# Kernel optimization log

Measured on AMD Instinct MI355X. Metric: run time of the kernel, lower is better.

## Reference

```python
import jax, jax.numpy as jnp
import numpy as np

EMPTY, TRUE, FALSE = 0.0, 1.0, 2.0  # MemoryVal ternary encoding

B = 2048          # batch
IN_BITS = 4096    # raw input bits
N_IN, N_ST, N_OUT = 2048, 1024, 1024
K = 14            # bits (connections) per neuron -> memory_size = 2**K
M = 2 ** K


def setup_inputs() -> dict:
    key = jax.random.key(0)
    ks = jax.random.split(key, 8)
    return {
        "input_bits": jax.random.randint(ks[0], (B, IN_BITS), 0, 2, dtype=jnp.int32),
        "state_bits": jax.random.randint(ks[1], (B, N_ST), 0, 2, dtype=jnp.int32),
        "in_conn": jax.random.randint(ks[2], (N_IN, K), 0, IN_BITS, dtype=jnp.int32),
        "in_mem": jax.random.randint(ks[3], (N_IN, M), 0, 3).astype(jnp.float32),
        "st_conn": jax.random.randint(ks[4], (N_ST, K), 0, N_IN + N_ST, dtype=jnp.int32),
        "st_mem": jax.random.randint(ks[5], (N_ST, M), 0, 3).astype(jnp.float32),
        "out_conn": jax.random.randint(ks[6], (N_OUT, K), 0, N_IN + N_ST, dtype=jnp.int32),
        "out_mem": jax.random.randint(ks[7], (N_OUT, M), 0, 3).astype(jnp.float32),
    }


def _ram_layer(bits, conn, mem):
    """bits: [B, T] 0/1; conn: [N, K] indices into T; mem: [N, 2**K] ternary."""
    k = conn.shape[1]
    g = bits[:, conn].astype(jnp.int32)                      # [B, N, K] gathered local bits
    w = (2 ** jnp.arange(k - 1, -1, -1)).astype(jnp.int32)   # MSB-first packing (matches _get_desired_bits)
    addr = jnp.sum(g * w, axis=-1)                           # [B, N] memory addresses
    vals = mem[jnp.arange(mem.shape[0])[None, :], addr]      # [B, N] per-neuron LUT lookup
    return jnp.where(vals == TRUE, 1.0, 0.0).astype(jnp.float32)  # neuron fires iff TRUE


def reference(input_bits, state_bits, in_conn, in_mem, st_conn, st_mem, out_conn, out_mem):
    h_in = _ram_layer(input_bits, in_conn, in_mem)                          # [B, N_IN]
    s_inp = jnp.concatenate([h_in, state_bits.astype(h_in.dtype)], axis=1)  # [B, N_IN+N_ST]
    s_out = _ram_layer(s_inp, st_conn, st_mem)                              # [B, N_ST]
    o_inp = jnp.concatenate([h_in, s_out], axis=1)                          # [B, N_IN+N_ST]
    return _ram_layer(o_inp, out_conn, out_mem)                             # [B, N_OUT]
```

## Files before the change

### kernel.cpp

```cpp
#include <hip/hip_runtime.h>
#include <stdint.h>

#define BATCH   2048
#define IN_BITS 4096
#define N_IN    2048
#define N_ST    1024
#define N_OUT   1024
#define KBITS   14
#define MW      512

#define BROW 128
#define PAD  129

#define IM_F 33554432L
#define SM_F 16777216L
#define OM_F 16777216L

__global__ __launch_bounds__(256) void pack_mem(const float* __restrict__ im,
                                                const float* __restrict__ sm,
                                                const float* __restrict__ om,
                                                uint32_t* __restrict__ dst) {
    int wid = (blockIdx.x * 256 + threadIdx.x) >> 6;
    int lane = threadIdx.x & 63;
    long f0 = (long)wid << 10;
    const float* s;
    long base;
    if (f0 < IM_F)              { s = im; base = f0; }
    else if (f0 < IM_F + SM_F)  { s = sm; base = f0 - IM_F; }
    else                        { s = om; base = f0 - (IM_F + SM_F); }
    unsigned long long m[16];
#pragma unroll
    for (int j = 0; j < 16; j++)
        m[j] = __ballot(s[base + j * 64 + lane] == 1.0f);
    if (lane == 0) {
        uint4* o = (uint4*)(dst + (f0 >> 5));
#pragma unroll
        for (int j = 0; j < 8; j++) {
            uint4 q;
            q.x = (uint32_t)m[2 * j];
            q.y = (uint32_t)(m[2 * j] >> 32);
            q.z = (uint32_t)m[2 * j + 1];
            q.w = (uint32_t)(m[2 * j + 1] >> 32);
            o[j] = q;
        }
    }
}

__global__ __launch_bounds__(256) void pack_in(const int* __restrict__ src,
                                               uint32_t* __restrict__ dst) {
    int wid = (blockIdx.x * 256 + threadIdx.x) >> 6;
    int lane = threadIdx.x & 63;
    long f0 = (long)wid << 10;
    unsigned long long m[16];
#pragma unroll
    for (int j = 0; j < 16; j++)
        m[j] = __ballot(src[f0 + j * 64 + lane] == 1);
    if (lane == 0) {
        uint4* o = (uint4*)(dst + (f0 >> 5));
#pragma unroll
        for (int j = 0; j < 8; j++) {
            uint4 q;
            q.x = (uint32_t)m[2 * j];
            q.y = (uint32_t)(m[2 * j] >> 32);
            q.z = (uint32_t)m[2 * j + 1];
            q.w = (uint32_t)(m[2 * j + 1] >> 32);
            o[j] = q;
        }
    }
}

__global__ __launch_bounds__(256) void pack_st(const int* __restrict__ src,
                                               uint32_t* __restrict__ buf) {
    int wid = (blockIdx.x * 256 + threadIdx.x) >> 6;
    int lane = threadIdx.x & 63;
    long f0 = (long)wid << 10;
    unsigned long long m[16];
#pragma unroll
    for (int j = 0; j < 16; j++)
        m[j] = __ballot(src[f0 + j * 64 + lane] == 1);
    if (lane == 0) {
        uint4* o = (uint4*)(buf + (long)wid * BROW + 64);
#pragma unroll
        for (int j = 0; j < 8; j++) {
            uint4 q;
            q.x = (uint32_t)m[2 * j];
            q.y = (uint32_t)(m[2 * j] >> 32);
            q.z = (uint32_t)m[2 * j + 1];
            q.w = (uint32_t)(m[2 * j + 1] >> 32);
            o[j] = q;
        }
    }
}

template <int NW, int MODE>
__global__ __launch_bounds__(256) void ram_layer(const uint32_t* __restrict__ src,
                                                 const int* __restrict__ conn,
                                                 const uint32_t* __restrict__ memp,
                                                 uint32_t* __restrict__ dst) {
    __shared__ uint32_t lds[64 * PAD];
    const int tid = threadIdx.x;
    const int b0 = blockIdx.y * 64;

    {
        const uint4* g = (const uint4*)(src + (long)b0 * BROW);
        for (int v = tid; v < 64 * BROW / 4; v += 256) {
            uint4 d = g[v];
            int row = v >> 5;
            int col = (v & 31) * 4;
            uint32_t* p = lds + row * PAD + col;
            p[0] = d.x; p[1] = d.y; p[2] = d.z; p[3] = d.w;
        }
    }
    __syncthreads();

    const int lane = tid & 63;
    const int wv = __builtin_amdgcn_readfirstlane(tid >> 6);
    const int n0 = blockIdx.x * (4 * NW) + wv * NW;
    const uint32_t* myrow = lds + lane * PAD;

    unsigned long long msk = 0;
#pragma unroll 2
    for (int i = 0; i < NW; ++i) {
        const int n = n0 + i;
        const int* c = conn + n * KBITS;
        uint32_t addr = 0;
#pragma unroll
        for (int k = 0; k < KBITS; k++) {
            int idx = c[k];
            int wd = idx >> 5;
            if (MODE == 2 && idx >= 2048) wd += 32;
            addr = (addr << 1) | ((myrow[wd] >> (idx & 31)) & 1u);
        }
        uint32_t v = memp[(long)n * MW + (addr >> 5)];
        unsigned long long m = __ballot(((v >> (addr & 31)) & 1u) != 0);
        msk = (lane == i) ? m : msk;
    }

    unsigned long long x = msk;
#define TSTEP(S, M)                                                         \
    {                                                                       \
        unsigned long long t =                                              \
            (unsigned long long)__shfl_xor((long long)x, S, 64);            \
        x = (lane & S) ? ((x & ~(M)) | ((t & ~(M)) >> S))                   \
                       : ((x & (M)) | ((t & (M)) << S));                    \
    }
    TSTEP(32, 0x00000000ffffffffULL)
    TSTEP(16, 0x0000ffff0000ffffULL)
    TSTEP(8,  0x00ff00ff00ff00ffULL)
    TSTEP(4,  0x0f0f0f0f0f0f0f0fULL)
    TSTEP(2,  0x3333333333333333ULL)
    TSTEP(1,  0x5555555555555555ULL)
#undef TSTEP

    if (MODE == 0) {
        *(uint32_t*)(dst + (long)(b0 + lane) * BROW + (n0 >> 5)) = (uint32_t)x;
    } else if (MODE == 1) {
        ((uint16_t*)(dst + (long)(b0 + lane) * BROW + 96))[n0 >> 4] = (uint16_t)x;
    } else {
        ((uint16_t*)(dst + (long)(b0 + lane) * 32))[n0 >> 4] = (uint16_t)x;
    }
}

__global__ __launch_bounds__(256) void expand_out(const uint32_t* __restrict__ pout,
                                                  float4* __restrict__ out) {
    int t = blockIdx.x * 256 + threadIdx.x;
    int b = t >> 8;
    int c4 = (t & 255) * 4;
    uint32_t w = pout[b * 32 + (c4 >> 5)];
    int sh = c4 & 31;
    float4 f;
    f.x = (float)((w >> (sh + 0)) & 1u);
    f.y = (float)((w >> (sh + 1)) & 1u);
    f.z = (float)((w >> (sh + 2)) & 1u);
    f.w = (float)((w >> (sh + 3)) & 1u);
    out[t] = f;
}

extern "C" void kernel_launch(void* const* d_in, const int* in_sizes, int n_in,
                              void* d_out, int out_size, void* d_ws, size_t ws_size,
                              hipStream_t stream) {
    const int*   input_bits = (const int*)d_in[0];
    const int*   state_bits = (const int*)d_in[1];
    const int*   in_conn    = (const int*)d_in[2];
    const float* in_mem     = (const float*)d_in[3];
    const int*   st_conn    = (const int*)d_in[4];
    const float* st_mem     = (const float*)d_in[5];
    const int*   out_conn   = (const int*)d_in[6];
    const float* out_mem    = (const float*)d_in[7];
    float*       out        = (float*)d_out;

    char* ws = (char*)d_ws;
    uint32_t* bits1 = (uint32_t*)(ws);
    uint32_t* buf   = (uint32_t*)(ws + 1048576);
    uint32_t* pout  = (uint32_t*)(ws + 2097152);
    uint32_t* tbl   = (uint32_t*)(ws + 2359296);
    uint32_t* im_p  = tbl;
    uint32_t* sm_p  = tbl + 1048576;
    uint32_t* om_p  = tbl + 1572864;

    pack_in<<<2048, 256, 0, stream>>>(input_bits, bits1);
    pack_st<<<512, 256, 0, stream>>>(state_bits, buf);
    pack_mem<<<16384, 256, 0, stream>>>(in_mem, st_mem, out_mem, tbl);

    ram_layer<32, 0><<<dim3(16, 32), 256, 0, stream>>>(bits1, in_conn, im_p, buf);
    ram_layer<16, 1><<<dim3(16, 32), 256, 0, stream>>>(buf, st_conn, sm_p, buf);
    ram_layer<16, 2><<<dim3(16, 32), 256, 0, stream>>>(buf, out_conn, om_p, pout);

    expand_out<<<2048, 256, 0, stream>>>(pout, (float4*)out);
}
```

Measured before the change: 370.9 us.

## Fuse pack kernels with vectorized loads, halve per-wave neurons, fold output expansion

Merges the three pack kernels into one launch that reads inputs and memory tables with 16-byte vector loads and combines nibbles through lane shuffles instead of per-element ballots. Each RAM layer now uses half as many neurons per wave over a grid twice as wide, which gives more blocks for occupancy. The last layer writes float outputs directly, removing the separate expand kernel and the packed output buffer. The packing stage is dominated by reading the large float memory tables, so it stays bandwidth-bound. The narrower ballots still use only the low lanes (16 and 8 bits), so the bit-transpose does redundant work.

```diff
diff --git a/kernel.cpp b/kernel.cpp
--- a/kernel.cpp
+++ b/kernel.cpp
@@ -2,92 +2,82 @@
 #include <stdint.h>
 
 #define BATCH   2048
-#define IN_BITS 4096
-#define N_IN    2048
-#define N_ST    1024
-#define N_OUT   1024
 #define KBITS   14
 #define MW      512
-
-#define BROW 128
-#define PAD  129
+#define BROW    128
+#define PAD     129
 
 #define IM_F 33554432L
 #define SM_F 16777216L
-#define OM_F 16777216L
 
-__global__ __launch_bounds__(256) void pack_mem(const float* __restrict__ im,
-                                                const float* __restrict__ sm,
-                                                const float* __restrict__ om,
-                                                uint32_t* __restrict__ dst) {
-    int wid = (blockIdx.x * 256 + threadIdx.x) >> 6;
-    int lane = threadIdx.x & 63;
-    long f0 = (long)wid << 10;
-    const float* s;
-    long base;
-    if (f0 < IM_F)              { s = im; base = f0; }
-    else if (f0 < IM_F + SM_F)  { s = sm; base = f0 - IM_F; }
-    else                        { s = om; base = f0 - (IM_F + SM_F); }
-    unsigned long long m[16];
+#define W_IN  4096
+#define W_ST  5120
+#define W_END 37888
+
+__global__ __launch_bounds__(256) void pack_all(
+    const int4* __restrict__ in_b, const int4* __restrict__ st_b,
+    const float4* __restrict__ im, const float4* __restrict__ sm,
+    const float4* __restrict__ om,
+    uint32_t* __restrict__ bits1, uint32_t* __restrict__ buf,
+    uint32_t* __restrict__ tbl) {
+    const int gw = (blockIdx.x * 256 + threadIdx.x) >> 6;
+    const int lane = threadIdx.x & 63;
+    uint32_t nib[8];
+    long wbase;
+    if (gw < W_ST) {
+        const int4* src;
+        long ebase;
+        if (gw < W_IN) { src = in_b; ebase = (long)gw << 11; }
+        else           { src = st_b; ebase = (long)(gw - W_IN) << 11; }
+        const int4* p = src + (ebase >> 2) + lane;
+        int4 r[8];
 #pragma unroll
-    for (int j = 0; j < 16; j++)
-        m[j] = __ballot(s[base + j * 64 + lane] == 1.0f);
-    if (lane == 0) {
-        uint4* o = (uint4*)(dst + (f0 >> 5));
+        for (int j = 0; j < 8; j++) r[j] = p[j * 64];
 #pragma unroll
-        for (int j = 0; j < 8; j++) {
-            uint4 q;
-            q.x = (uint32_t)m[2 * j];
-            q.y = (uint32_t)(m[2 * j] >> 32);
-            q.z = (uint32_t)m[2 * j + 1];
-            q.w = (uint32_t)(m[2 * j + 1] >> 32);
-            o[j] = q;
-        }
+        for (int j = 0; j < 8; j++)
+            nib[j] = (uint32_t)(r[j].x == 1) | ((uint32_t)(r[j].y == 1) << 1) |
+                     ((uint32_t)(r[j].z == 1) << 2) | ((uint32_t)(r[j].w == 1) << 3);
+        wbase = ebase >> 5;
+    } else {
+        long fbase = (long)(gw - W_ST) << 11;
+        const float4* src;
+        long eb;
+        if (fbase < IM_F)             { src = im; eb = fbase; }
+        else if (fbase < IM_F + SM_F) { src = sm; eb = fbase - IM_F; }
+        else                          { src = om; eb = fbase - IM_F - SM_F; }
+        const float4* p = src + (eb >> 2) + lane;
+        float4 r[8];
+#pragma unroll
+        for (int j = 0; j < 8; j++) r[j] = p[j * 64];
+#pragma unroll
+        for (int j = 0; j < 8; j++)
+            nib[j] = (uint32_t)(r[j].x == 1.0f) | ((uint32_t)(r[j].y == 1.0f) << 1) |
+                     ((uint32_t)(r[j].z == 1.0f) << 2) | ((uint32_t)(r[j].w == 1.0f) << 3);
+        wbase = fbase >> 5;
     }
-}
-
-__global__ __launch_bounds__(256) void pack_in(const int* __restrict__ src,
-                                               uint32_t* __restrict__ dst) {
-    int wid = (blockIdx.x * 256 + threadIdx.x) >> 6;
-    int lane = threadIdx.x & 63;
-    long f0 = (long)wid << 10;
-    unsigned long long m[16];
+    uint32_t w[8];
 #pragma unroll
-    for (int j = 0; j < 16; j++)
-        m[j] = __ballot(src[f0 + j * 64 + lane] == 1);
-    if (lane == 0) {
-        uint4* o = (uint4*)(dst + (f0 >> 5));
+    for (int j = 0; j < 8; j++) {
+        uint32_t x = nib[j] << (4 * (lane & 7));
+        x |= __shfl_xor(x, 1, 64);
+        x |= __shfl_xor(x, 2, 64);
+        x |= __shfl_xor(x, 4, 64);
+        w[j] = x;
+    }
+    if ((lane & 7) == 0) {
+        const int s = lane >> 3;
+        if (gw < W_IN) {
 #pragma unroll
-        for (int j = 0; j < 8; j++) {
-            uint4 q;
-            q.x = (uint32_t)m[2 * j];
-            q.y = (uint32_t)(m[2 * j] >> 32);
-            q.z = (uint32_t)m[2 * j + 1];
-            q.w = (uint32_t)(m[2 * j + 1] >> 32);
-            o[j] = q;
-        }
-    }
-}
-
-__global__ __launch_bounds__(256) void pack_st(const int* __restrict__ src,
-                                               uint32_t* __restrict__ buf) {
-    int wid = (blockIdx.x * 256 + threadIdx.x) >> 6;
-    int lane = threadIdx.x & 63;
-    long f0 = (long)wid << 10;
-    unsigned long long m[16];
+            for (int j = 0; j < 8; j++) bits1[wbase + j * 8 + s] = w[j];
+        } else if (gw < W_ST) {
 #pragma unroll
-    for (int j = 0; j < 16; j++)
-        m[j] = __ballot(src[f0 + j * 64 + lane] == 1);
-    if (lane == 0) {
-        uint4* o = (uint4*)(buf + (long)wid * BROW + 64);
+            for (int j = 0; j < 8; j++) {
+                long g = wbase + j * 8 + s;
+                buf[(g >> 5) * BROW + 64 + (g & 31)] = w[j];
+            }
+        } else {
 #pragma unroll
-        for (int j = 0; j < 8; j++) {
-            uint4 q;
-            q.x = (uint32_t)m[2 * j];
-            q.y = (uint32_t)(m[2 * j] >> 32);
-            q.z = (uint32_t)m[2 * j + 1];
-            q.w = (uint32_t)(m[2 * j + 1] >> 32);
-            o[j] = q;
+            for (int j = 0; j < 8; j++) tbl[wbase + j * 8 + s] = w[j];
         }
     }
 }
@@ -96,11 +86,11 @@
 __global__ __launch_bounds__(256) void ram_layer(const uint32_t* __restrict__ src,
                                                  const int* __restrict__ conn,
                                                  const uint32_t* __restrict__ memp,
-                                                 uint32_t* __restrict__ dst) {
+                                                 uint32_t* __restrict__ dst,
+                                                 float* __restrict__ fout) {
     __shared__ uint32_t lds[64 * PAD];
     const int tid = threadIdx.x;
     const int b0 = blockIdx.y * 64;
-
     {
         const uint4* g = (const uint4*)(src + (long)b0 * BROW);
         for (int v = tid; v < 64 * BROW / 4; v += 256) {
@@ -153,27 +143,19 @@
 #undef TSTEP
 
     if (MODE == 0) {
-        *(uint32_t*)(dst + (long)(b0 + lane) * BROW + (n0 >> 5)) = (uint32_t)x;
+        ((uint16_t*)(dst + (long)(b0 + lane) * BROW))[n0 >> 4] = (uint16_t)x;
     } else if (MODE == 1) {
-        ((uint16_t*)(dst + (long)(b0 + lane) * BROW + 96))[n0 >> 4] = (uint16_t)x;
+        ((uint8_t*)(dst + (long)(b0 + lane) * BROW + 96))[n0 >> 3] = (uint8_t)x;
     } else {
-        ((uint16_t*)(dst + (long)(b0 + lane) * 32))[n0 >> 4] = (uint16_t)x;
+        float* o = fout + (long)(b0 + lane) * 1024 + n0;
+        float4 f0, f1;
+        f0.x = (float)((x >> 0) & 1); f0.y = (float)((x >> 1) & 1);
+        f0.z = (float)((x >> 2) & 1); f0.w = (float)((x >> 3) & 1);
+        f1.x = (float)((x >> 4) & 1); f1.y = (float)((x >> 5) & 1);
+        f1.z = (float)((x >> 6) & 1); f1.w = (float)((x >> 7) & 1);
+        ((float4*)o)[0] = f0;
+        ((float4*)o)[1] = f1;
     }
-}
-
-__global__ __launch_bounds__(256) void expand_out(const uint32_t* __restrict__ pout,
-                                                  float4* __restrict__ out) {
-    int t = blockIdx.x * 256 + threadIdx.x;
-    int b = t >> 8;
-    int c4 = (t & 255) * 4;
-    uint32_t w = pout[b * 32 + (c4 >> 5)];
-    int sh = c4 & 31;
-    float4 f;
-    f.x = (float)((w >> (sh + 0)) & 1u);
-    f.y = (float)((w >> (sh + 1)) & 1u);
-    f.z = (float)((w >> (sh + 2)) & 1u);
-    f.w = (float)((w >> (sh + 3)) & 1u);
-    out[t] = f;
 }
 
 extern "C" void kernel_launch(void* const* d_in, const int* in_sizes, int n_in,
@@ -192,19 +174,17 @@
     char* ws = (char*)d_ws;
     uint32_t* bits1 = (uint32_t*)(ws);
     uint32_t* buf   = (uint32_t*)(ws + 1048576);
-    uint32_t* pout  = (uint32_t*)(ws + 2097152);
-    uint32_t* tbl   = (uint32_t*)(ws + 2359296);
+    uint32_t* tbl   = (uint32_t*)(ws + 2097152);
     uint32_t* im_p  = tbl;
     uint32_t* sm_p  = tbl + 1048576;
     uint32_t* om_p  = tbl + 1572864;
 
-    pack_in<<<2048, 256, 0, stream>>>(input_bits, bits1);
-    pack_st<<<512, 256, 0, stream>>>(state_bits, buf);
-    pack_mem<<<16384, 256, 0, stream>>>(in_mem, st_mem, out_mem, tbl);
+    pack_all<<<W_END / 4, 256, 0, stream>>>(
+        (const int4*)input_bits, (const int4*)state_bits,
+        (const float4*)in_mem, (const float4*)st_mem, (const float4*)out_mem,
+        bits1, buf, tbl);
 
-    ram_layer<32, 0><<<dim3(16, 32), 256, 0, stream>>>(bits1, in_conn, im_p, buf);
-    ram_layer<16, 1><<<dim3(16, 32), 256, 0, stream>>>(buf, st_conn, sm_p, buf);
-    ram_layer<16, 2><<<dim3(16, 32), 256, 0, stream>>>(buf, out_conn, om_p, pout);
-
-    expand_out<<<2048, 256, 0, stream>>>(pout, (float4*)out);
+    ram_layer<16, 0><<<dim3(32, 32), 256, 0, stream>>>(bits1, in_conn, im_p, buf, nullptr);
+    ram_layer<8, 1><<<dim3(32, 32), 256, 0, stream>>>(buf, st_conn, sm_p, buf, nullptr);
+    ram_layer<8, 2><<<dim3(32, 32), 256, 0, stream>>>(buf, out_conn, om_p, nullptr, out);
 }
```

Result: faster. 350.5 us (-5.5%).
